# Kernel tuning notes

Measured on AMD Instinct MI355X. Metric: run time of the kernel, lower is better.

Reference implementation:

```python
import jax, jax.numpy as jnp
import numpy as np

HEADS = 16
DIM_HEAD = 64
SCALE = DIM_HEAD ** -0.5


def setup_inputs() -> dict:
    key = jax.random.key(0)
    k1, k2, k3 = jax.random.split(key, 3)
    B, N, D = 4, 8192, 1024
    inner = HEADS * DIM_HEAD  # 1024
    x = jax.random.normal(k1, (B, N, D), dtype=jnp.float32)
    w_qkv = jax.random.normal(k2, (D, 3 * inner), dtype=jnp.float32) * (D ** -0.5)
    w_out = jax.random.normal(k3, (inner, D), dtype=jnp.float32) * (inner ** -0.5)
    b_out = jnp.zeros((D,), dtype=jnp.float32)
    return {"x": x, "w_qkv": w_qkv, "w_out": w_out, "b_out": b_out}


def reference(x, w_qkv, w_out, b_out):
    B, N, D = x.shape
    h, d = HEADS, DIM_HEAD
    qkv = x @ w_qkv  # [B, N, 3*h*d]
    q, k, v = jnp.split(qkv, 3, axis=-1)

    def to_heads(t):  # b n (h d) -> (b h) n d
        return t.reshape(B, N, h, d).transpose(0, 2, 1, 3).reshape(B * h, N, d)

    q, k, v = map(to_heads, (q, k, v))
    q = jax.nn.softmax(q * SCALE, axis=-1)   # softmax over feature dim
    k = jax.nn.softmax(k, axis=-2)           # softmax over sequence dim
    # context = q^T k per head: [bh, d, e]
    context = jnp.einsum('bnd,bne->bde', q, k)
    # out[b,n,e] = sum_d context[b,d,e] * v[b,n,d]
    out = jnp.einsum('bde,bnd->bne', context, v)
    out = out.reshape(B, h, N, d).transpose(0, 2, 1, 3).reshape(B, N, h * d)
    return out @ w_out + b_out
```

## Files before the change

kernel.cpp:

```cpp
#include <hip/hip_runtime.h>

typedef unsigned short u16;
typedef __attribute__((ext_vector_type(8))) short short8;
typedef __attribute__((ext_vector_type(4))) unsigned short u16x4;
typedef __attribute__((ext_vector_type(8))) __bf16 bf16x8;
typedef __attribute__((ext_vector_type(4))) float f32x4;

#define B_SZ 4
#define NSEQ 8192
#define DMODEL 1024
#define MROWS 32768
#define QKVCOLS 3072

static __device__ __forceinline__ u16 f2bf(float f) {
  unsigned u = __builtin_bit_cast(unsigned, f);
  u += 0x7fffu + ((u >> 16) & 1u);
  return (u16)(u >> 16);
}
static __device__ __forceinline__ float bf2f(u16 h) {
  return __builtin_bit_cast(float, ((unsigned)h) << 16);
}
static __device__ __forceinline__ void gload16(const u16* g, u16* l) {
  __builtin_amdgcn_global_load_lds(
      (const __attribute__((address_space(1))) unsigned*)g,
      (__attribute__((address_space(3))) unsigned*)l, 16, 0, 0);
}

__global__ __launch_bounds__(256) void k_convert(const float* __restrict__ in,
                                                 u16* __restrict__ out, long n) {
  long i = ((long)blockIdx.x * 256 + threadIdx.x) * 4;
  if (i >= n) return;
  f32x4 v = *(const f32x4*)(in + i);
  u16x4 o;
  o[0] = f2bf(v[0]); o[1] = f2bf(v[1]); o[2] = f2bf(v[2]); o[3] = f2bf(v[3]);
  *(u16x4*)(out + i) = o;
}

__global__ __launch_bounds__(256) void k_cv(const float* __restrict__ wq,
                                            u16* __restrict__ wvb) {
  int idx = (blockIdx.x * 256 + threadIdx.x) * 4;
  int i = idx >> 10, k = idx & 1023;
  f32x4 v = *(const f32x4*)(wq + (long)i * QKVCOLS + 2048 + k);
  u16x4 o;
  o[0] = f2bf(v[0]); o[1] = f2bf(v[1]); o[2] = f2bf(v[2]); o[3] = f2bf(v[3]);
  *(u16x4*)(wvb + idx) = o;
}

__global__ __launch_bounds__(256) void k_transpose(const float* __restrict__ in,
                                                   u16* __restrict__ out, int R, int C) {
  __shared__ float tile[32][33];
  int c0 = blockIdx.x * 32, r0 = blockIdx.y * 32;
  int tx = threadIdx.x, ty = threadIdx.y;
#pragma unroll
  for (int j = 0; j < 32; j += 8)
    tile[ty + j][tx] = in[(long)(r0 + ty + j) * C + c0 + tx];
  __syncthreads();
#pragma unroll
  for (int j = 0; j < 32; j += 8)
    out[(long)(c0 + ty + j) * R + r0 + tx] = f2bf(tile[tx][ty + j]);
}

#define MFMA_QUAD(Qm, Qn, A_, B_)                                              \
  _Pragma("unroll") for (int m = 0; m < 4; ++m)                                \
  _Pragma("unroll") for (int n = 0; n < 2; ++n)                                \
    acc[Qm][Qn][m][n] = __builtin_amdgcn_mfma_f32_16x16x32_bf16(A_[m][1], B_[n][1], \
        __builtin_amdgcn_mfma_f32_16x16x32_bf16(A_[m][0], B_[n][0], acc[Qm][Qn][m][n], 0, 0, 0), 0, 0, 0);

template <int EPI, int K, int LDA, int NBN, int LDC, long BSTR>
__global__ __launch_bounds__(512, 2) void k_gemm256(
    const u16* __restrict__ A, const u16* __restrict__ Bp,
    const float* __restrict__ bias, u16* __restrict__ qh,
    u16* __restrict__ kh, float* __restrict__ Cf, float* __restrict__ S) {
  __shared__ __align__(16) u16 sm[65536];
  const int t = threadIdx.x;
  const int lane = t & 63;
  const int w = t >> 6;
  const int wq = w >> 2;
  const int wn = w & 3;
  const int lr = lane & 15;
  const int hi = lane >> 4;
  const int l3 = lane >> 3;

  const int nwg = gridDim.x;
  const int bid = blockIdx.x;
  const int swz = (bid & 7) * (nwg >> 3) + (bid >> 3);
  const int per = 8 * NBN;
  const int grp = swz / per, rem = swz % per;
  const int bm = grp * 8 + (rem & 7);
  const int bn = rem / 8;

  const u16* B = Bp + (long)(bm >> 5) * BSTR;
  const int gcol = ((lane & 7) ^ l3) * 8;

  auto stA = [&](int tile, int half, int buf) {
    u16* dst = &sm[buf * 16384 + (half * 128 + w * 16) * 64];
    const u16* g = A + ((long)(bm * 256 + half * 128 + w * 16 + l3)) * LDA + tile * 64 + gcol;
    gload16(g, dst);
    gload16(g + 8 * (long)LDA, dst + 8 * 64);
  };
  auto stB = [&](int tile, int half, int buf) {
#pragma unroll
    for (int L = 0; L < 2; ++L) {
      int base = half * 128 + w * 16 + L * 8;
      int grow = bn * 256 + ((base >> 5) & 3) * 64 + half * 32 + (base & 31) + l3;
      const u16* g = B + (long)grow * K + tile * 64 + gcol;
      gload16(g, &sm[32768 + buf * 16384 + base * 64]);
    }
  };

  const int su = (lr & 7) << 3;
  const int cu0 = (hi * 8) ^ su;
  const int cu1 = (32 + hi * 8) ^ su;
  const int arow = wq * 64 + lr;
  const int brow = wn * 32 + lr;

  auto ldA = [&](int buf, int Qm, int m, int kk) -> bf16x8 {
    return *(const bf16x8*)&sm[buf * 16384 + (Qm * 128 + arow + m * 16) * 64 + (kk ? cu1 : cu0)];
  };
  auto ldB = [&](int buf, int Qn, int n, int kk) -> bf16x8 {
    return *(const bf16x8*)&sm[32768 + buf * 16384 + (Qn * 128 + brow + n * 16) * 64 + (kk ? cu1 : cu0)];
  };

  f32x4 acc[2][2][4][2] = {};
  bf16x8 af[4][2], af2[4][2], bl[2][2], bh[2][2];
  constexpr int NT = K >> 6;

  stA(0, 0, 0); stB(0, 0, 0); stB(0, 1, 0); stA(0, 1, 0);
  stA(1, 0, 1); stB(1, 0, 1); stB(1, 1, 1);
  asm volatile("s_waitcnt vmcnt(6)" ::: "memory");
  __builtin_amdgcn_s_barrier();

  auto tile_body = [&](int tt, int s1, int s2) {
    const int p = tt & 1;
#pragma unroll
    for (int m = 0; m < 4; ++m) { af[m][0] = ldA(p, 0, m, 0); af[m][1] = ldA(p, 0, m, 1); }
#pragma unroll
    for (int n = 0; n < 2; ++n) { bl[n][0] = ldB(p, 0, n, 0); bl[n][1] = ldB(p, 0, n, 1); }
    __builtin_amdgcn_sched_barrier(0);
#pragma unroll
    for (int n = 0; n < 2; ++n) { bh[n][0] = ldB(p, 1, n, 0); bh[n][1] = ldB(p, 1, n, 1); }
    __builtin_amdgcn_sched_barrier(0);
    if (s1) stA(tt + 1, 1, 1 - p);
    __builtin_amdgcn_sched_barrier(0);
    asm volatile("s_waitcnt lgkmcnt(4)" ::: "memory");
    __builtin_amdgcn_sched_barrier(0);
    __builtin_amdgcn_s_setprio(1);
    MFMA_QUAD(0, 0, af, bl)
    __builtin_amdgcn_s_setprio(0);
    __builtin_amdgcn_s_barrier();
#pragma unroll
    for (int m = 0; m < 4; ++m) { af2[m][0] = ldA(p, 1, m, 0); af2[m][1] = ldA(p, 1, m, 1); }
    __builtin_amdgcn_sched_barrier(0);
    if (s2) stA(tt + 2, 0, p);
    __builtin_amdgcn_sched_barrier(0);
    asm volatile("s_waitcnt lgkmcnt(8)" ::: "memory");
    __builtin_amdgcn_sched_barrier(0);
    __builtin_amdgcn_s_setprio(1);
    MFMA_QUAD(0, 1, af, bh)
    __builtin_amdgcn_s_setprio(0);
    __builtin_amdgcn_s_barrier();
    if (s2) { stB(tt + 2, 0, p); stB(tt + 2, 1, p); }
    __builtin_amdgcn_sched_barrier(0);
    asm volatile("s_waitcnt lgkmcnt(0)" ::: "memory");
    __builtin_amdgcn_sched_barrier(0);
    __builtin_amdgcn_s_setprio(1);
    MFMA_QUAD(1, 1, af2, bh)
    MFMA_QUAD(1, 0, af2, bl)
    __builtin_amdgcn_s_setprio(0);
    if (s2) { asm volatile("s_waitcnt vmcnt(6)" ::: "memory"); }
    else if (s1) { asm volatile("s_waitcnt vmcnt(0)" ::: "memory"); }
    __builtin_amdgcn_s_barrier();
  };

  for (int tt = 0; tt < NT - 2; ++tt) tile_body(tt, 1, 1);
  tile_body(NT - 2, 1, 0);
  tile_body(NT - 1, 0, 0);

  const int row0 = bm * 256 + wq * 64 + hi * 4;
  const int colw = bn * 256 + wn * 64;

  if (EPI == 1) {
#pragma unroll
    for (int Qm = 0; Qm < 2; ++Qm)
#pragma unroll
      for (int m = 0; m < 4; ++m)
#pragma unroll
        for (int r = 0; r < 4; ++r) {
          long row = row0 + Qm * 128 + m * 16 + r;
#pragma unroll
          for (int Qn = 0; Qn < 2; ++Qn)
#pragma unroll
            for (int n = 0; n < 2; ++n) {
              int col = colw + Qn * 32 + n * 16 + lr;
              Cf[row * LDC + col] = acc[Qm][Qn][m][n][r] + bias[col];
            }
        }
    return;
  }

  if (bn < 4) {
    const int h = bn * 4 + wn;
#pragma unroll
    for (int Qm = 0; Qm < 2; ++Qm)
#pragma unroll
      for (int m = 0; m < 4; ++m)
#pragma unroll
        for (int r = 0; r < 4; ++r) {
          float pv[2][2];
          float mx = -1e30f;
#pragma unroll
          for (int Qn = 0; Qn < 2; ++Qn)
#pragma unroll
            for (int nn = 0; nn < 2; ++nn) {
              pv[Qn][nn] = acc[Qm][Qn][m][nn][r] * 0.125f;
              mx = fmaxf(mx, pv[Qn][nn]);
            }
#pragma unroll
          for (int off = 1; off < 16; off <<= 1) mx = fmaxf(mx, __shfl_xor(mx, off));
          float s = 0.f;
#pragma unroll
          for (int Qn = 0; Qn < 2; ++Qn)
#pragma unroll
            for (int nn = 0; nn < 2; ++nn) { pv[Qn][nn] = __expf(pv[Qn][nn] - mx); s += pv[Qn][nn]; }
#pragma unroll
          for (int off = 1; off < 16; off <<= 1) s += __shfl_xor(s, off);
          float inv = 1.0f / s;
          long row = row0 + Qm * 128 + m * 16 + r;
          long base = (((long)(row >> 13) * 16 + h) * NSEQ + (row & 8191)) * 64;
#pragma unroll
          for (int Qn = 0; Qn < 2; ++Qn)
#pragma unroll
            for (int nn = 0; nn < 2; ++nn)
              qh[base + Qn * 32 + nn * 16 + lr] = f2bf(pv[Qn][nn] * inv);
        }
  } else {
    const int h = (bn - 4) * 4 + wn;
    float cs[2][2] = {};
#pragma unroll
    for (int Qm = 0; Qm < 2; ++Qm)
#pragma unroll
      for (int m = 0; m < 4; ++m)
#pragma unroll
        for (int r = 0; r < 4; ++r) {
          long row = row0 + Qm * 128 + m * 16 + r;
          long base = (((long)(row >> 13) * 16 + h) * NSEQ + (row & 8191)) * 64;
#pragma unroll
          for (int Qn = 0; Qn < 2; ++Qn)
#pragma unroll
            for (int nn = 0; nn < 2; ++nn) {
              float pe = __expf(acc[Qm][Qn][m][nn][r]);
              cs[Qn][nn] += pe;
              kh[base + Qn * 32 + nn * 16 + lr] = f2bf(pe);
            }
        }
#pragma unroll
    for (int Qn = 0; Qn < 2; ++Qn)
#pragma unroll
      for (int nn = 0; nn < 2; ++nn) {
        cs[Qn][nn] += __shfl_xor(cs[Qn][nn], 16);
        cs[Qn][nn] += __shfl_xor(cs[Qn][nn], 32);
      }
    if (lane < 16) {
      int b = bm >> 5;
#pragma unroll
      for (int Qn = 0; Qn < 2; ++Qn)
#pragma unroll
        for (int nn = 0; nn < 2; ++nn)
          atomicAdd(&S[b * DMODEL + h * 64 + Qn * 32 + nn * 16 + lane], cs[Qn][nn]);
    }
  }
}

__global__ __launch_bounds__(256) void k_ctx(const u16* __restrict__ qhat,
                                             const u16* __restrict__ khat,
                                             float* __restrict__ ctx_part) {
  __shared__ __align__(16) u16 smu[2 * 17408];
  const int bh = blockIdx.x, nc = blockIdx.y;
  const int t = threadIdx.x;
  const int lane = t & 63;
  const int ww = t >> 6;
  const int lr = lane & 15;
  const int hi = lane >> 4;

  const int isK = t >> 7;
  const int u = t & 127;
  const int ng = u >> 3;
  const int dc = u & 7;
  const u16* srcm = (isK ? khat : qhat) + (long)bh * NSEQ * 64;

  f32x4 acc[4][4] = {};
  short8 v[8];

  auto load_stage = [&](int s) {
    long nb = (long)nc * 1024 + s * 128;
    const u16* src = srcm + (nb + ng * 8) * 64 + dc * 8;
#pragma unroll
    for (int i = 0; i < 8; ++i) v[i] = *(const short8*)(src + i * 64);
  };
  auto write_stage = [&](int s) {
    const int buf = s & 1;
    u16* dst0 = &smu[buf * 17408 + isK * 8704 + (dc * 8) * 136 + (ng ^ dc) * 8];
#pragma unroll
    for (int j = 0; j < 8; ++j) {
      short8 o;
#pragma unroll
      for (int i = 0; i < 8; ++i) o[i] = v[i][j];
      *(short8*)(dst0 + j * 136) = o;
    }
  };
  auto compute = [&](int s) {
    const int buf = s & 1;
    const int g = ww * 4 + hi;
    const u16* qb = &smu[buf * 17408];
    const u16* kb = qb + 8704;
    bf16x8 a[4], b[4];
#pragma unroll
    for (int dt = 0; dt < 4; ++dt) {
      int d = dt * 16 + lr;
      a[dt] = *(const bf16x8*)(qb + d * 136 + (g ^ ((d >> 3) & 7)) * 8);
    }
#pragma unroll
    for (int et = 0; et < 4; ++et) {
      int d = et * 16 + lr;
      b[et] = *(const bf16x8*)(kb + d * 136 + (g ^ ((d >> 3) & 7)) * 8);
    }
#pragma unroll
    for (int dt = 0; dt < 4; ++dt)
#pragma unroll
      for (int et = 0; et < 4; ++et)
        acc[dt][et] = __builtin_amdgcn_mfma_f32_16x16x32_bf16(a[dt], b[et], acc[dt][et], 0, 0, 0);
  };

  load_stage(0);
  write_stage(0);
  __syncthreads();
  for (int s = 0; s < 8; ++s) {
    if (s < 7) load_stage(s + 1);
    compute(s);
    if (s < 7) write_stage(s + 1);
    __syncthreads();
  }

  float* smf = (float*)smu;
#pragma unroll
  for (int dt = 0; dt < 4; ++dt)
#pragma unroll
    for (int et = 0; et < 4; ++et)
      *(f32x4*)&smf[ww * 4096 + (dt * 4 + hi) * 256 + (et * 16 + lr) * 4] = acc[dt][et];
  __syncthreads();
  float* op = ctx_part + ((long)nc * 64 + bh) * 4096;
#pragma unroll
  for (int rep = 0; rep < 4; ++rep) {
    int p4 = rep * 1024 + t * 4;
    f32x4 sum = *(const f32x4*)&smf[p4];
    sum += *(const f32x4*)&smf[4096 + p4];
    sum += *(const f32x4*)&smf[8192 + p4];
    sum += *(const f32x4*)&smf[12288 + p4];
    *(f32x4*)&op[p4] = sum;
  }
}

__global__ __launch_bounds__(256) void k_cred(const float* __restrict__ ctx_part,
                                              const float* __restrict__ S,
                                              u16* __restrict__ ctxn) {
  const int bh = blockIdx.x;
  const int b = bh >> 4, h = bh & 15;
  const int p = blockIdx.y * 256 + threadIdx.x;
  float s = 0.f;
#pragma unroll
  for (int nc = 0; nc < 8; ++nc)
    s += ctx_part[((long)nc * 64 + bh) * 4096 + p];
  int d = (p >> 8) * 4 + (p & 3);
  int e = (p >> 2) & 63;
  ctxn[(long)bh * 4096 + d * 64 + e] = f2bf(s / S[b * DMODEL + h * 64 + e]);
}

__global__ __launch_bounds__(256) void k_ct(const u16* __restrict__ woutT,
                                            const u16* __restrict__ ctxn,
                                            u16* __restrict__ ctT) {
  __shared__ __align__(16) u16 cb[64 * 72];
  const int b = blockIdx.x, h = blockIdx.y;
  const int t = threadIdx.x, lane = t & 63, ww = t >> 6;
  const int lr = lane & 15, hi = lane >> 4;
  {
    const u16* src = ctxn + ((long)(b * 16 + h)) * 4096 + t * 16;
    int row = t >> 2, col = (t & 3) * 16;
    *(short8*)(cb + row * 72 + col) = *(const short8*)src;
    *(short8*)(cb + row * 72 + col + 8) = *(const short8*)(src + 8);
  }
  __syncthreads();
  bf16x8 bfrag[4][2];
#pragma unroll
  for (int n = 0; n < 4; ++n)
#pragma unroll
    for (int kk = 0; kk < 2; ++kk)
      bfrag[n][kk] = *(const bf16x8*)(cb + (n * 16 + lr) * 72 + kk * 32 + hi * 8);
  const int row0 = ww * 256;
  u16* outp = ctT + ((long)b * 1024) * 1024 + (long)h * 64;
#pragma unroll
  for (int m = 0; m < 16; ++m) {
    int arow = row0 + m * 16 + lr;
    const u16* ap = woutT + (long)arow * DMODEL + h * 64;
    bf16x8 a0 = *(const bf16x8*)(ap + hi * 8);
    bf16x8 a1 = *(const bf16x8*)(ap + 32 + hi * 8);
    f32x4 accr[4] = {};
#pragma unroll
    for (int n = 0; n < 4; ++n)
      accr[n] = __builtin_amdgcn_mfma_f32_16x16x32_bf16(a1, bfrag[n][1],
                __builtin_amdgcn_mfma_f32_16x16x32_bf16(a0, bfrag[n][0], accr[n], 0, 0, 0), 0, 0, 0);
#pragma unroll
    for (int n = 0; n < 4; ++n)
#pragma unroll
      for (int r = 0; r < 4; ++r)
        outp[(long)(row0 + m * 16 + hi * 4 + r) * DMODEL + n * 16 + lr] = f2bf(accr[n][r]);
  }
}

__global__ __launch_bounds__(256) void k_wc(const u16* __restrict__ A,
                                            const u16* __restrict__ B,
                                            u16* __restrict__ Cb) {
  __shared__ __align__(16) u16 As[128 * 32];
  __shared__ __align__(16) u16 Bs[128 * 32];
  const int K = 1024, ldc = 1024;
  const int t = threadIdx.x;
  const int lane = t & 63;
  const int w = t >> 6;
  const int wm = w >> 1, wn = w & 1;
  const long bm = blockIdx.x, bn = blockIdx.y;

  f32x4 acc[4][4] = {};

  const u16* Ag = A + bm * 128 * (long)K;
  const u16* Bg = B + bn * 128 * (long)K;
  const int r0 = t >> 2;
  const int s0 = (t & 3) * 8;
  const int ko = (lane >> 4) * 8;
  const int lr = lane & 15;

  for (int kt = 0; kt < K; kt += 32) {
    short8 a0 = *(const short8*)(Ag + (long)r0 * K + kt + s0);
    short8 a1 = *(const short8*)(Ag + (long)(r0 + 64) * K + kt + s0);
    short8 b0 = *(const short8*)(Bg + (long)r0 * K + kt + s0);
    short8 b1 = *(const short8*)(Bg + (long)(r0 + 64) * K + kt + s0);
    __syncthreads();
    *(short8*)(As + r0 * 32 + s0) = a0;
    *(short8*)(As + (r0 + 64) * 32 + s0) = a1;
    *(short8*)(Bs + r0 * 32 + s0) = b0;
    *(short8*)(Bs + (r0 + 64) * 32 + s0) = b1;
    __syncthreads();
    bf16x8 af[4], bfr[4];
#pragma unroll
    for (int m = 0; m < 4; ++m)
      af[m] = *(const bf16x8*)(As + (wm * 64 + m * 16 + lr) * 32 + ko);
#pragma unroll
    for (int n = 0; n < 4; ++n)
      bfr[n] = *(const bf16x8*)(Bs + (wn * 64 + n * 16 + lr) * 32 + ko);
#pragma unroll
    for (int m = 0; m < 4; ++m)
#pragma unroll
      for (int n = 0; n < 4; ++n)
        acc[m][n] = __builtin_amdgcn_mfma_f32_16x16x32_bf16(af[m], bfr[n], acc[m][n], 0, 0, 0);
  }

  const int row_base = (int)bm * 128 + wm * 64 + (lane >> 4) * 4;
  const int col_base = (int)bn * 128 + wn * 64 + lr;
#pragma unroll
  for (int m = 0; m < 4; ++m)
#pragma unroll
    for (int n = 0; n < 4; ++n)
#pragma unroll
      for (int r = 0; r < 4; ++r)
        Cb[(long)(row_base + m * 16 + r) * ldc + col_base + n * 16] = f2bf(acc[m][n][r]);
}

extern "C" void kernel_launch(void* const* d_in, const int* in_sizes, int n_in,
                              void* d_out, int out_size, void* d_ws, size_t ws_size,
                              hipStream_t stream) {
  const float* x = (const float*)d_in[0];
  const float* w_qkv = (const float*)d_in[1];
  const float* w_out = (const float*)d_in[2];
  const float* b_out = (const float*)d_in[3];
  float* out = (float*)d_out;
  char* ws = (char*)d_ws;

  u16* xb      = (u16*)(ws + 0);
  u16* wqkvT   = (u16*)(ws + 67108864L);
  u16* woutT   = (u16*)(ws + 73400320L);
  u16* wvb     = (u16*)(ws + 75497472L);
  u16* qhat    = (u16*)(ws + 77594624L);
  u16* khat    = (u16*)(ws + 144703488L);
  float* S     = (float*)(ws + 211812352L);
  u16* ctxn    = (u16*)(ws + 211828736L);
  float* cpart = (float*)(ws + 212353024L);
  u16* ctT     = (u16*)(ws + 220741632L);
  u16* wcT     = (u16*)(ws + 229130240L);

  hipMemsetAsync(S, 0, 16384, stream);

  k_convert<<<32768, 256, 0, stream>>>(x, xb, (long)MROWS * DMODEL);
  k_cv<<<1024, 256, 0, stream>>>(w_qkv, wvb);
  k_transpose<<<dim3(64, 32), dim3(32, 8), 0, stream>>>(w_qkv, wqkvT, DMODEL, QKVCOLS);
  k_transpose<<<dim3(32, 32), dim3(32, 8), 0, stream>>>(w_out, woutT, DMODEL, DMODEL);

  k_gemm256<0, DMODEL, DMODEL, 8, QKVCOLS, 0L>
      <<<dim3((MROWS / 256) * (2048 / 256)), 512, 0, stream>>>(
      xb, wqkvT, nullptr, qhat, khat, nullptr, S);

  k_ctx<<<dim3(64, 8), 256, 0, stream>>>(qhat, khat, cpart);
  k_cred<<<dim3(64, 16), 256, 0, stream>>>(cpart, S, ctxn);
  k_ct<<<dim3(4, 16), 256, 0, stream>>>(woutT, ctxn, ctT);
  k_wc<<<dim3(32, 8), 256, 0, stream>>>(ctT, wvb, wcT);

  k_gemm256<1, DMODEL, DMODEL, 4, DMODEL, (long)DMODEL * DMODEL>
      <<<dim3((MROWS / 256) * (DMODEL / 256)), 512, 0, stream>>>(
      xb, wcT, b_out, nullptr, nullptr, out, nullptr);
}
```

Baseline: 331.8 us.

## Fuse Q/K softmax and context accumulation into the QK GEMM epilogue

The QK projection kernel now computes both the Q and K tiles for the same rows and heads in one block using two sequential GEMM passes. Its epilogue applies the softmaxes, stages normalized q and exp(k) in shared memory, and computes per-slice partial context matrices with MFMA. This removes the large qhat/khat round trip to global memory and the separate k_ctx kernel. In exchange the kernel keeps two accumulator sets, which raises register pressure and may cut occupancy, and k_cred must now reduce 32 partial slices instead of 8.

New measurement: 399.2 us. 20.3% more time.

```diff
diff --git a/kernel.cpp b/kernel.cpp
--- a/kernel.cpp
+++ b/kernel.cpp
@@ -66,12 +66,11 @@
     acc[Qm][Qn][m][n] = __builtin_amdgcn_mfma_f32_16x16x32_bf16(A_[m][1], B_[n][1], \
         __builtin_amdgcn_mfma_f32_16x16x32_bf16(A_[m][0], B_[n][0], acc[Qm][Qn][m][n], 0, 0, 0), 0, 0, 0);
 
-template <int EPI, int K, int LDA, int NBN, int LDC, long BSTR>
-__global__ __launch_bounds__(512, 2) void k_gemm256(
+__global__ __launch_bounds__(512, 2) void k_gemmqk(
     const u16* __restrict__ A, const u16* __restrict__ Bp,
-    const float* __restrict__ bias, u16* __restrict__ qh,
-    u16* __restrict__ kh, float* __restrict__ Cf, float* __restrict__ S) {
+    float* __restrict__ cpart, float* __restrict__ S) {
   __shared__ __align__(16) u16 sm[65536];
+  constexpr int K = 1024, LDA = 1024;
   const int t = threadIdx.x;
   const int lane = t & 63;
   const int w = t >> 6;
@@ -84,13 +83,13 @@
   const int nwg = gridDim.x;
   const int bid = blockIdx.x;
   const int swz = (bid & 7) * (nwg >> 3) + (bid >> 3);
-  const int per = 8 * NBN;
+  const int per = 8 * 4;
   const int grp = swz / per, rem = swz % per;
   const int bm = grp * 8 + (rem & 7);
-  const int bn = rem / 8;
-
-  const u16* B = Bp + (long)(bm >> 5) * BSTR;
+  const int hn = rem / 8;
+
   const int gcol = ((lane & 7) ^ l3) * 8;
+  int bnn = hn;
 
   auto stA = [&](int tile, int half, int buf) {
     u16* dst = &sm[buf * 16384 + (half * 128 + w * 16) * 64];
@@ -102,8 +101,8 @@
 #pragma unroll
     for (int L = 0; L < 2; ++L) {
       int base = half * 128 + w * 16 + L * 8;
-      int grow = bn * 256 + ((base >> 5) & 3) * 64 + half * 32 + (base & 31) + l3;
-      const u16* g = B + (long)grow * K + tile * 64 + gcol;
+      int grow = bnn * 256 + ((base >> 5) & 3) * 64 + half * 32 + (base & 31) + l3;
+      const u16* g = Bp + (long)grow * K + tile * 64 + gcol;
       gload16(g, &sm[32768 + buf * 16384 + base * 64]);
     }
   };
@@ -121,16 +120,12 @@
     return *(const bf16x8*)&sm[32768 + buf * 16384 + (Qn * 128 + brow + n * 16) * 64 + (kk ? cu1 : cu0)];
   };
 
-  f32x4 acc[2][2][4][2] = {};
+  f32x4 accq[2][2][4][2] = {};
+  f32x4 acck[2][2][4][2] = {};
   bf16x8 af[4][2], af2[4][2], bl[2][2], bh[2][2];
   constexpr int NT = K >> 6;
 
-  stA(0, 0, 0); stB(0, 0, 0); stB(0, 1, 0); stA(0, 1, 0);
-  stA(1, 0, 1); stB(1, 0, 1); stB(1, 1, 1);
-  asm volatile("s_waitcnt vmcnt(6)" ::: "memory");
-  __builtin_amdgcn_s_barrier();
-
-  auto tile_body = [&](int tt, int s1, int s2) {
+  auto tile_body = [&](int tt, int s1, int s2, f32x4 (&acc)[2][2][4][2]) {
     const int p = tt & 1;
 #pragma unroll
     for (int m = 0; m < 4; ++m) { af[m][0] = ldA(p, 0, m, 0); af[m][1] = ldA(p, 0, m, 1); }
@@ -172,204 +167,131 @@
     __builtin_amdgcn_s_barrier();
   };
 
-  for (int tt = 0; tt < NT - 2; ++tt) tile_body(tt, 1, 1);
-  tile_body(NT - 2, 1, 0);
-  tile_body(NT - 1, 0, 0);
-
-  const int row0 = bm * 256 + wq * 64 + hi * 4;
-  const int colw = bn * 256 + wn * 64;
-
-  if (EPI == 1) {
-#pragma unroll
-    for (int Qm = 0; Qm < 2; ++Qm)
-#pragma unroll
-      for (int m = 0; m < 4; ++m)
-#pragma unroll
-        for (int r = 0; r < 4; ++r) {
-          long row = row0 + Qm * 128 + m * 16 + r;
+  auto run_pass = [&](f32x4 (&acc)[2][2][4][2]) {
+    stA(0, 0, 0); stB(0, 0, 0); stB(0, 1, 0); stA(0, 1, 0);
+    stA(1, 0, 1); stB(1, 0, 1); stB(1, 1, 1);
+    asm volatile("s_waitcnt vmcnt(6)" ::: "memory");
+    __builtin_amdgcn_s_barrier();
+    for (int tt = 0; tt < NT - 2; ++tt) tile_body(tt, 1, 1, acc);
+    tile_body(NT - 2, 1, 0, acc);
+    tile_body(NT - 1, 0, 0, acc);
+  };
+
+  bnn = hn;      run_pass(accq);
+  bnn = 4 + hn;  run_pass(acck);
+
+  const int b = bm >> 5;
+  const int slice = bm & 31;
+  const int swlo = lr & 7;
+
+#pragma unroll
+  for (int R = 0; R < 2; ++R) {
+    __syncthreads();
+    if ((wn >> 1) == R) {
+      const int pp = wn & 1;
+      u16* qplane = sm + pp * 32768;
+      u16* kplane = qplane + 16384;
+      const int h = hn * 4 + wn;
+      float cs[2][2] = {};
+#pragma unroll
+      for (int Qm = 0; Qm < 2; ++Qm)
+#pragma unroll
+        for (int m = 0; m < 4; ++m) {
+          u16x4 q4[2][2], k4[2][2];
+#pragma unroll
+          for (int r = 0; r < 4; ++r) {
+            float pv[2][2], mx = -1e30f;
+#pragma unroll
+            for (int Qn = 0; Qn < 2; ++Qn)
+#pragma unroll
+              for (int nn = 0; nn < 2; ++nn) {
+                pv[Qn][nn] = accq[Qm][Qn][m][nn][r] * 0.125f;
+                mx = fmaxf(mx, pv[Qn][nn]);
+              }
+#pragma unroll
+            for (int off = 1; off < 16; off <<= 1) mx = fmaxf(mx, __shfl_xor(mx, off));
+            float s = 0.f;
+#pragma unroll
+            for (int Qn = 0; Qn < 2; ++Qn)
+#pragma unroll
+              for (int nn = 0; nn < 2; ++nn) { pv[Qn][nn] = __expf(pv[Qn][nn] - mx); s += pv[Qn][nn]; }
+#pragma unroll
+            for (int off = 1; off < 16; off <<= 1) s += __shfl_xor(s, off);
+            float inv = 1.0f / s;
+#pragma unroll
+            for (int Qn = 0; Qn < 2; ++Qn)
+#pragma unroll
+              for (int nn = 0; nn < 2; ++nn) {
+                q4[Qn][nn][r] = f2bf(pv[Qn][nn] * inv);
+                float pe = __expf(acck[Qm][Qn][m][nn][r]);
+                cs[Qn][nn] += pe;
+                k4[Qn][nn][r] = f2bf(pe);
+              }
+          }
+          const int blk = wq * 8 + Qm * 16 + m * 2 + (hi >> 1);
+          const int halfo = (hi & 1) << 2;
 #pragma unroll
           for (int Qn = 0; Qn < 2; ++Qn)
 #pragma unroll
-            for (int n = 0; n < 2; ++n) {
-              int col = colw + Qn * 32 + n * 16 + lr;
-              Cf[row * LDC + col] = acc[Qm][Qn][m][n][r] + bias[col];
+            for (int nn = 0; nn < 2; ++nn) {
+              int d = Qn * 32 + nn * 16 + lr;
+              int idx = d * 256 + ((blk ^ (d & 7)) << 3) + halfo;
+              *(u16x4*)&qplane[idx] = q4[Qn][nn];
+              *(u16x4*)&kplane[idx] = k4[Qn][nn];
             }
         }
-    return;
-  }
-
-  if (bn < 4) {
-    const int h = bn * 4 + wn;
-#pragma unroll
-    for (int Qm = 0; Qm < 2; ++Qm)
-#pragma unroll
-      for (int m = 0; m < 4; ++m)
-#pragma unroll
-        for (int r = 0; r < 4; ++r) {
-          float pv[2][2];
-          float mx = -1e30f;
-#pragma unroll
-          for (int Qn = 0; Qn < 2; ++Qn)
-#pragma unroll
-            for (int nn = 0; nn < 2; ++nn) {
-              pv[Qn][nn] = acc[Qm][Qn][m][nn][r] * 0.125f;
-              mx = fmaxf(mx, pv[Qn][nn]);
-            }
-#pragma unroll
-          for (int off = 1; off < 16; off <<= 1) mx = fmaxf(mx, __shfl_xor(mx, off));
-          float s = 0.f;
-#pragma unroll
-          for (int Qn = 0; Qn < 2; ++Qn)
-#pragma unroll
-            for (int nn = 0; nn < 2; ++nn) { pv[Qn][nn] = __expf(pv[Qn][nn] - mx); s += pv[Qn][nn]; }
-#pragma unroll
-          for (int off = 1; off < 16; off <<= 1) s += __shfl_xor(s, off);
-          float inv = 1.0f / s;
-          long row = row0 + Qm * 128 + m * 16 + r;
-          long base = (((long)(row >> 13) * 16 + h) * NSEQ + (row & 8191)) * 64;
-#pragma unroll
-          for (int Qn = 0; Qn < 2; ++Qn)
-#pragma unroll
-            for (int nn = 0; nn < 2; ++nn)
-              qh[base + Qn * 32 + nn * 16 + lr] = f2bf(pv[Qn][nn] * inv);
+#pragma unroll
+      for (int Qn = 0; Qn < 2; ++Qn)
+#pragma unroll
+        for (int nn = 0; nn < 2; ++nn) {
+          cs[Qn][nn] += __shfl_xor(cs[Qn][nn], 16);
+          cs[Qn][nn] += __shfl_xor(cs[Qn][nn], 32);
         }
-  } else {
-    const int h = (bn - 4) * 4 + wn;
-    float cs[2][2] = {};
-#pragma unroll
-    for (int Qm = 0; Qm < 2; ++Qm)
-#pragma unroll
-      for (int m = 0; m < 4; ++m)
-#pragma unroll
-        for (int r = 0; r < 4; ++r) {
-          long row = row0 + Qm * 128 + m * 16 + r;
-          long base = (((long)(row >> 13) * 16 + h) * NSEQ + (row & 8191)) * 64;
-#pragma unroll
-          for (int Qn = 0; Qn < 2; ++Qn)
-#pragma unroll
-            for (int nn = 0; nn < 2; ++nn) {
-              float pe = __expf(acc[Qm][Qn][m][nn][r]);
-              cs[Qn][nn] += pe;
-              kh[base + Qn * 32 + nn * 16 + lr] = f2bf(pe);
-            }
+      if (lane < 16) {
+#pragma unroll
+        for (int Qn = 0; Qn < 2; ++Qn)
+#pragma unroll
+          for (int nn = 0; nn < 2; ++nn)
+            atomicAdd(&S[b * DMODEL + h * 64 + Qn * 32 + nn * 16 + lane], cs[Qn][nn]);
+      }
+    }
+    __syncthreads();
+    {
+      const int pp = w & 1;
+      const int q = w >> 1;
+      const u16* qb = sm + pp * 32768;
+      const u16* kb = qb + 16384;
+      f32x4 ca[4] = {};
+#pragma unroll
+      for (int nc = 0; nc < 8; ++nc) {
+        int blkr = (nc * 4 + hi) ^ swlo;
+        bf16x8 a = *(const bf16x8*)&qb[(q * 16 + lr) * 256 + (blkr << 3)];
+#pragma unroll
+        for (int et = 0; et < 4; ++et) {
+          bf16x8 bfr = *(const bf16x8*)&kb[(et * 16 + lr) * 256 + (blkr << 3)];
+          ca[et] = __builtin_amdgcn_mfma_f32_16x16x32_bf16(a, bfr, ca[et], 0, 0, 0);
         }
-#pragma unroll
-    for (int Qn = 0; Qn < 2; ++Qn)
-#pragma unroll
-      for (int nn = 0; nn < 2; ++nn) {
-        cs[Qn][nn] += __shfl_xor(cs[Qn][nn], 16);
-        cs[Qn][nn] += __shfl_xor(cs[Qn][nn], 32);
       }
-    if (lane < 16) {
-      int b = bm >> 5;
-#pragma unroll
-      for (int Qn = 0; Qn < 2; ++Qn)
-#pragma unroll
-        for (int nn = 0; nn < 2; ++nn)
-          atomicAdd(&S[b * DMODEL + h * 64 + Qn * 32 + nn * 16 + lane], cs[Qn][nn]);
+      const int hl = 2 * R + (w & 1);
+      const long bh = (long)b * 16 + hn * 4 + hl;
+      float* op = cpart + ((long)slice * 64 + bh) * 4096 + (q * 4 + hi) * 256 + lr * 4;
+#pragma unroll
+      for (int et = 0; et < 4; ++et)
+        *(f32x4*)(op + et * 64) = ca[et];
     }
   }
 }
 
-__global__ __launch_bounds__(256) void k_ctx(const u16* __restrict__ qhat,
-                                             const u16* __restrict__ khat,
-                                             float* __restrict__ ctx_part) {
-  __shared__ __align__(16) u16 smu[2 * 17408];
-  const int bh = blockIdx.x, nc = blockIdx.y;
-  const int t = threadIdx.x;
-  const int lane = t & 63;
-  const int ww = t >> 6;
-  const int lr = lane & 15;
-  const int hi = lane >> 4;
-
-  const int isK = t >> 7;
-  const int u = t & 127;
-  const int ng = u >> 3;
-  const int dc = u & 7;
-  const u16* srcm = (isK ? khat : qhat) + (long)bh * NSEQ * 64;
-
-  f32x4 acc[4][4] = {};
-  short8 v[8];
-
-  auto load_stage = [&](int s) {
-    long nb = (long)nc * 1024 + s * 128;
-    const u16* src = srcm + (nb + ng * 8) * 64 + dc * 8;
-#pragma unroll
-    for (int i = 0; i < 8; ++i) v[i] = *(const short8*)(src + i * 64);
-  };
-  auto write_stage = [&](int s) {
-    const int buf = s & 1;
-    u16* dst0 = &smu[buf * 17408 + isK * 8704 + (dc * 8) * 136 + (ng ^ dc) * 8];
-#pragma unroll
-    for (int j = 0; j < 8; ++j) {
-      short8 o;
-#pragma unroll
-      for (int i = 0; i < 8; ++i) o[i] = v[i][j];
-      *(short8*)(dst0 + j * 136) = o;
-    }
-  };
-  auto compute = [&](int s) {
-    const int buf = s & 1;
-    const int g = ww * 4 + hi;
-    const u16* qb = &smu[buf * 17408];
-    const u16* kb = qb + 8704;
-    bf16x8 a[4], b[4];
-#pragma unroll
-    for (int dt = 0; dt < 4; ++dt) {
-      int d = dt * 16 + lr;
-      a[dt] = *(const bf16x8*)(qb + d * 136 + (g ^ ((d >> 3) & 7)) * 8);
-    }
-#pragma unroll
-    for (int et = 0; et < 4; ++et) {
-      int d = et * 16 + lr;
-      b[et] = *(const bf16x8*)(kb + d * 136 + (g ^ ((d >> 3) & 7)) * 8);
-    }
-#pragma unroll
-    for (int dt = 0; dt < 4; ++dt)
-#pragma unroll
-      for (int et = 0; et < 4; ++et)
-        acc[dt][et] = __builtin_amdgcn_mfma_f32_16x16x32_bf16(a[dt], b[et], acc[dt][et], 0, 0, 0);
-  };
-
-  load_stage(0);
-  write_stage(0);
-  __syncthreads();
-  for (int s = 0; s < 8; ++s) {
-    if (s < 7) load_stage(s + 1);
-    compute(s);
-    if (s < 7) write_stage(s + 1);
-    __syncthreads();
-  }
-
-  float* smf = (float*)smu;
-#pragma unroll
-  for (int dt = 0; dt < 4; ++dt)
-#pragma unroll
-    for (int et = 0; et < 4; ++et)
-      *(f32x4*)&smf[ww * 4096 + (dt * 4 + hi) * 256 + (et * 16 + lr) * 4] = acc[dt][et];
-  __syncthreads();
-  float* op = ctx_part + ((long)nc * 64 + bh) * 4096;
-#pragma unroll
-  for (int rep = 0; rep < 4; ++rep) {
-    int p4 = rep * 1024 + t * 4;
-    f32x4 sum = *(const f32x4*)&smf[p4];
-    sum += *(const f32x4*)&smf[4096 + p4];
-    sum += *(const f32x4*)&smf[8192 + p4];
-    sum += *(const f32x4*)&smf[12288 + p4];
-    *(f32x4*)&op[p4] = sum;
-  }
-}
-
-__global__ __launch_bounds__(256) void k_cred(const float* __restrict__ ctx_part,
+__global__ __launch_bounds__(256) void k_cred(const float* __restrict__ cpart,
                                               const float* __restrict__ S,
                                               u16* __restrict__ ctxn) {
   const int bh = blockIdx.x;
   const int b = bh >> 4, h = bh & 15;
   const int p = blockIdx.y * 256 + threadIdx.x;
   float s = 0.f;
-#pragma unroll
-  for (int nc = 0; nc < 8; ++nc)
-    s += ctx_part[((long)nc * 64 + bh) * 4096 + p];
+#pragma unroll 8
+  for (int sl = 0; sl < 32; ++sl)
+    s += cpart[((long)sl * 64 + bh) * 4096 + p];
   int d = (p >> 8) * 4 + (p & 3);
   int e = (p >> 2) & 63;
   ctxn[(long)bh * 4096 + d * 64 + e] = f2bf(s / S[b * DMODEL + h * 64 + e]);
@@ -473,6 +395,134 @@
         Cb[(long)(row_base + m * 16 + r) * ldc + col_base + n * 16] = f2bf(acc[m][n][r]);
 }
 
+template <int K, int LDA, int NBN, int LDC, long BSTR>
+__global__ __launch_bounds__(512, 2) void k_gemmout(
+    const u16* __restrict__ A, const u16* __restrict__ Bp,
+    const float* __restrict__ bias, float* __restrict__ Cf) {
+  __shared__ __align__(16) u16 sm[65536];
+  const int t = threadIdx.x;
+  const int lane = t & 63;
+  const int w = t >> 6;
+  const int wq = w >> 2;
+  const int wn = w & 3;
+  const int lr = lane & 15;
+  const int hi = lane >> 4;
+  const int l3 = lane >> 3;
+
+  const int nwg = gridDim.x;
+  const int bid = blockIdx.x;
+  const int swz = (bid & 7) * (nwg >> 3) + (bid >> 3);
+  const int per = 8 * NBN;
+  const int grp = swz / per, rem = swz % per;
+  const int bm = grp * 8 + (rem & 7);
+  const int bn = rem / 8;
+
+  const u16* B = Bp + (long)(bm >> 5) * BSTR;
+  const int gcol = ((lane & 7) ^ l3) * 8;
+
+  auto stA = [&](int tile, int half, int buf) {
+    u16* dst = &sm[buf * 16384 + (half * 128 + w * 16) * 64];
+    const u16* g = A + ((long)(bm * 256 + half * 128 + w * 16 + l3)) * LDA + tile * 64 + gcol;
+    gload16(g, dst);
+    gload16(g + 8 * (long)LDA, dst + 8 * 64);
+  };
+  auto stB = [&](int tile, int half, int buf) {
+#pragma unroll
+    for (int L = 0; L < 2; ++L) {
+      int base = half * 128 + w * 16 + L * 8;
+      int grow = bn * 256 + ((base >> 5) & 3) * 64 + half * 32 + (base & 31) + l3;
+      const u16* g = B + (long)grow * K + tile * 64 + gcol;
+      gload16(g, &sm[32768 + buf * 16384 + base * 64]);
+    }
+  };
+
+  const int su = (lr & 7) << 3;
+  const int cu0 = (hi * 8) ^ su;
+  const int cu1 = (32 + hi * 8) ^ su;
+  const int arow = wq * 64 + lr;
+  const int brow = wn * 32 + lr;
+
+  auto ldA = [&](int buf, int Qm, int m, int kk) -> bf16x8 {
+    return *(const bf16x8*)&sm[buf * 16384 + (Qm * 128 + arow + m * 16) * 64 + (kk ? cu1 : cu0)];
+  };
+  auto ldB = [&](int buf, int Qn, int n, int kk) -> bf16x8 {
+    return *(const bf16x8*)&sm[32768 + buf * 16384 + (Qn * 128 + brow + n * 16) * 64 + (kk ? cu1 : cu0)];
+  };
+
+  f32x4 acc[2][2][4][2] = {};
+  bf16x8 af[4][2], af2[4][2], bl[2][2], bh[2][2];
+  constexpr int NT = K >> 6;
+
+  stA(0, 0, 0); stB(0, 0, 0); stB(0, 1, 0); stA(0, 1, 0);
+  stA(1, 0, 1); stB(1, 0, 1); stB(1, 1, 1);
+  asm volatile("s_waitcnt vmcnt(6)" ::: "memory");
+  __builtin_amdgcn_s_barrier();
+
+  auto tile_body = [&](int tt, int s1, int s2) {
+    const int p = tt & 1;
+#pragma unroll
+    for (int m = 0; m < 4; ++m) { af[m][0] = ldA(p, 0, m, 0); af[m][1] = ldA(p, 0, m, 1); }
+#pragma unroll
+    for (int n = 0; n < 2; ++n) { bl[n][0] = ldB(p, 0, n, 0); bl[n][1] = ldB(p, 0, n, 1); }
+    __builtin_amdgcn_sched_barrier(0);
+#pragma unroll
+    for (int n = 0; n < 2; ++n) { bh[n][0] = ldB(p, 1, n, 0); bh[n][1] = ldB(p, 1, n, 1); }
+    __builtin_amdgcn_sched_barrier(0);
+    if (s1) stA(tt + 1, 1, 1 - p);
+    __builtin_amdgcn_sched_barrier(0);
+    asm volatile("s_waitcnt lgkmcnt(4)" ::: "memory");
+    __builtin_amdgcn_sched_barrier(0);
+    __builtin_amdgcn_s_setprio(1);
+    MFMA_QUAD(0, 0, af, bl)
+    __builtin_amdgcn_s_setprio(0);
+    __builtin_amdgcn_s_barrier();
+#pragma unroll
+    for (int m = 0; m < 4; ++m) { af2[m][0] = ldA(p, 1, m, 0); af2[m][1] = ldA(p, 1, m, 1); }
+    __builtin_amdgcn_sched_barrier(0);
+    if (s2) stA(tt + 2, 0, p);
+    __builtin_amdgcn_sched_barrier(0);
+    asm volatile("s_waitcnt lgkmcnt(8)" ::: "memory");
+    __builtin_amdgcn_sched_barrier(0);
+    __builtin_amdgcn_s_setprio(1);
+    MFMA_QUAD(0, 1, af, bh)
+    __builtin_amdgcn_s_setprio(0);
+    __builtin_amdgcn_s_barrier();
+    if (s2) { stB(tt + 2, 0, p); stB(tt + 2, 1, p); }
+    __builtin_amdgcn_sched_barrier(0);
+    asm volatile("s_waitcnt lgkmcnt(0)" ::: "memory");
+    __builtin_amdgcn_sched_barrier(0);
+    __builtin_amdgcn_s_setprio(1);
+    MFMA_QUAD(1, 1, af2, bh)
+    MFMA_QUAD(1, 0, af2, bl)
+    __builtin_amdgcn_s_setprio(0);
+    if (s2) { asm volatile("s_waitcnt vmcnt(6)" ::: "memory"); }
+    else if (s1) { asm volatile("s_waitcnt vmcnt(0)" ::: "memory"); }
+    __builtin_amdgcn_s_barrier();
+  };
+
+  for (int tt = 0; tt < NT - 2; ++tt) tile_body(tt, 1, 1);
+  tile_body(NT - 2, 1, 0);
+  tile_body(NT - 1, 0, 0);
+
+  const int row0 = bm * 256 + wq * 64 + hi * 4;
+  const int colw = bn * 256 + wn * 64;
+#pragma unroll
+  for (int Qm = 0; Qm < 2; ++Qm)
+#pragma unroll
+    for (int m = 0; m < 4; ++m)
+#pragma unroll
+      for (int r = 0; r < 4; ++r) {
+        long row = row0 + Qm * 128 + m * 16 + r;
+#pragma unroll
+        for (int Qn = 0; Qn < 2; ++Qn)
+#pragma unroll
+          for (int n = 0; n < 2; ++n) {
+            int col = colw + Qn * 32 + n * 16 + lr;
+            Cf[row * LDC + col] = acc[Qm][Qn][m][n][r] + bias[col];
+          }
+      }
+}
+
 extern "C" void kernel_launch(void* const* d_in, const int* in_sizes, int n_in,
                               void* d_out, int out_size, void* d_ws, size_t ws_size,
                               hipStream_t stream) {
@@ -487,13 +537,11 @@
   u16* wqkvT   = (u16*)(ws + 67108864L);
   u16* woutT   = (u16*)(ws + 73400320L);
   u16* wvb     = (u16*)(ws + 75497472L);
-  u16* qhat    = (u16*)(ws + 77594624L);
-  u16* khat    = (u16*)(ws + 144703488L);
-  float* S     = (float*)(ws + 211812352L);
-  u16* ctxn    = (u16*)(ws + 211828736L);
-  float* cpart = (float*)(ws + 212353024L);
-  u16* ctT     = (u16*)(ws + 220741632L);
-  u16* wcT     = (u16*)(ws + 229130240L);
+  float* S     = (float*)(ws + 77594624L);
+  u16* ctxn    = (u16*)(ws + 77611008L);
+  float* cpart = (float*)(ws + 78135296L);
+  u16* ctT     = (u16*)(ws + 111689728L);
+  u16* wcT     = (u16*)(ws + 120078336L);
 
   hipMemsetAsync(S, 0, 16384, stream);
 
@@ -502,16 +550,13 @@
   k_transpose<<<dim3(64, 32), dim3(32, 8), 0, stream>>>(w_qkv, wqkvT, DMODEL, QKVCOLS);
   k_transpose<<<dim3(32, 32), dim3(32, 8), 0, stream>>>(w_out, woutT, DMODEL, DMODEL);
 
-  k_gemm256<0, DMODEL, DMODEL, 8, QKVCOLS, 0L>
-      <<<dim3((MROWS / 256) * (2048 / 256)), 512, 0, stream>>>(
-      xb, wqkvT, nullptr, qhat, khat, nullptr, S);
-
-  k_ctx<<<dim3(64, 8), 256, 0, stream>>>(qhat, khat, cpart);
+  k_gemmqk<<<dim3(512), 512, 0, stream>>>(xb, wqkvT, cpart, S);
+
   k_cred<<<dim3(64, 16), 256, 0, stream>>>(cpart, S, ctxn);
   k_ct<<<dim3(4, 16), 256, 0, stream>>>(woutT, ctxn, ctT);
   k_wc<<<dim3(32, 8), 256, 0, stream>>>(ctT, wvb, wcT);
 
-  k_gemm256<1, DMODEL, DMODEL, 4, DMODEL, (long)DMODEL * DMODEL>
+  k_gemmout<DMODEL, DMODEL, 4, DMODEL, (long)DMODEL * DMODEL>
       <<<dim3((MROWS / 256) * (DMODEL / 256)), 512, 0, stream>>>(
-      xb, wcT, b_out, nullptr, nullptr, out, nullptr);
-}
+      xb, wcT, b_out, out);
+}
```
